# Kernel tuning notes

Hardware: AMD Instinct MI355X
Metric: run time of the kernel (lower is better)

## Reference

```python
import jax, jax.numpy as jnp
import numpy as np

E = 1024
H = 16
DH = E // H
LN_EPS = 1e-5


def setup_inputs() -> dict:
    key = jax.random.key(0)
    ks = jax.random.split(key, 9)
    B, Lq, Lk = 8, 1024, 1024
    s = 0.02
    return {
        "query": jax.random.normal(ks[0], (B, Lq, E), jnp.float32),
        "key_t": jax.random.normal(ks[1], (B, Lk, E), jnp.float32),
        "value": jax.random.normal(ks[2], (B, Lk, E), jnp.float32),
        "in_proj_w": jax.random.normal(ks[3], (3 * E, E), jnp.float32) * s,
        "in_proj_b": jnp.zeros((3 * E,), jnp.float32),
        "out_proj_w": jax.random.normal(ks[4], (E, E), jnp.float32) * s,
        "out_proj_b": jnp.zeros((E,), jnp.float32),
        "ln_gamma": jnp.ones((E,), jnp.float32),
        "ln_beta": jnp.zeros((E,), jnp.float32),
    }


def _mha_cross(query, key_t, value, in_proj_w, in_proj_b, out_proj_w, out_proj_b,
               ln_gamma, ln_beta):
    B, Lq, _ = query.shape
    Lk = key_t.shape[1]
    wq, wk, wv = in_proj_w[:E], in_proj_w[E:2 * E], in_proj_w[2 * E:]
    bq, bk, bv = in_proj_b[:E], in_proj_b[E:2 * E], in_proj_b[2 * E:]
    # projections (torch Linear: x @ W^T + b)
    q = (query @ wq.T + bq).reshape(B, Lq, H, DH)
    k = (key_t @ wk.T + bk).reshape(B, Lk, H, DH)
    v = (value @ wv.T + bv).reshape(B, Lk, H, DH)
    scale = 1.0 / np.sqrt(DH).astype(np.float32)
    # unfused attention: explicit [B,H,Lq,Lk] scores (need_weights=True path)
    scores = jnp.einsum("bqhd,bkhd->bhqk", q, k) * scale
    probs = jax.nn.softmax(scores, axis=-1)
    attn = jnp.einsum("bhqk,bkhd->bqhd", probs, v).reshape(B, Lq, E)
    attn_out = attn @ out_proj_w.T + out_proj_b
    # averaged attention weights (average_attn_weights=True default)
    attn_weights = probs.mean(axis=1)  # [B, Lq, Lk]
    # residual + LayerNorm
    x = query + attn_out
    mu = x.mean(axis=-1, keepdims=True)
    var = x.var(axis=-1, keepdims=True)
    y = (x - mu) * jax.lax.rsqrt(var + LN_EPS) * ln_gamma + ln_beta
    return y, attn_weights


def reference(query, key_t, value, in_proj_w, in_proj_b, out_proj_w, out_proj_b,
              ln_gamma, ln_beta):
    return _mha_cross(query, key_t, value, in_proj_w, in_proj_b,
                      out_proj_w, out_proj_b, ln_gamma, ln_beta)
```

## Files before the change

kernel.cpp:

```cpp
#include <hip/hip_runtime.h>
#include <stdint.h>

#define E_DIM 1024
#define H_NUM 16
#define B_NUM 8
#define LQ 1024
#define LK 1024
#define MROWS (B_NUM * LQ)

typedef unsigned short u16;
typedef __attribute__((ext_vector_type(8))) short bf16x8;
typedef __attribute__((ext_vector_type(4))) short bf16x4;
typedef __attribute__((ext_vector_type(4))) float f32x4;
typedef __attribute__((ext_vector_type(2))) unsigned int u32x2;
typedef bf16x8 __attribute__((may_alias)) bf16x8_ma;
typedef bf16x4 __attribute__((may_alias)) bf16x4_ma;
typedef f32x4 __attribute__((may_alias)) f32x4_ma;
typedef u32x2 __attribute__((may_alias)) u32x2_ma;

typedef __attribute__((address_space(1))) const void* gas_ptr;
typedef __attribute__((address_space(3))) void* las_ptr;

__device__ __forceinline__ void gload16(const void* g, void* l) {
  __builtin_amdgcn_global_load_lds((gas_ptr)g, (las_ptr)l, 16, 0, 0);
}

__device__ __forceinline__ u16 f2bf(float f) {
  union { float f; uint32_t u; } c; c.f = f;
  return (u16)((c.u + 0x7FFFu + ((c.u >> 16) & 1u)) >> 16);
}

__device__ __forceinline__ uint32_t pack2bf(float lo, float hi) {
  return __builtin_amdgcn_perm(__float_as_uint(hi), __float_as_uint(lo), 0x07060302u);
}

#define MFMA_BF16(a, b, c) __builtin_amdgcn_mfma_f32_16x16x32_bf16((a), (b), (c), 0, 0, 0)

#define SCALE_Q 0.18033688011112042f


__global__ __launch_bounds__(256) void cvt_f32_bf16(const float* __restrict__ src,
                                                    u16* __restrict__ dst, int n4) {
  int i = blockIdx.x * 256 + threadIdx.x;
  const int stride = gridDim.x * 256;
  for (; i < n4; i += stride) {
    float4 v = ((const float4*)src)[i];
    ushort4 o;
    o.x = f2bf(v.x); o.y = f2bf(v.y); o.z = f2bf(v.z); o.w = f2bf(v.w);
    ((ushort4*)dst)[i] = o;
  }
}

__global__ __launch_bounds__(256) void cvt3_f32_bf16(
    const float* __restrict__ a0, const float* __restrict__ a1, const float* __restrict__ a2,
    u16* __restrict__ o0, u16* __restrict__ o1, u16* __restrict__ o2, int n4) {
  const float* s = (blockIdx.y == 0) ? a0 : (blockIdx.y == 1 ? a1 : a2);
  u16* d = (blockIdx.y == 0) ? o0 : (blockIdx.y == 1 ? o1 : o2);
  int i = blockIdx.x * 256 + threadIdx.x;
  const int stride = gridDim.x * 256;
  for (; i < n4; i += stride) {
    float4 v = ((const float4*)s)[i];
    ushort4 o;
    o.x = f2bf(v.x); o.y = f2bf(v.y); o.z = f2bf(v.z); o.w = f2bf(v.w);
    ((ushort4*)d)[i] = o;
  }
}


#define BAR() __builtin_amdgcn_s_barrier()
#define LGKM0() do { asm volatile("s_waitcnt lgkmcnt(0)" ::: "memory"); \
                     __builtin_amdgcn_sched_barrier(0); } while (0)
#define LGKM8() asm volatile("s_waitcnt lgkmcnt(8)" ::: "memory")
#define VMC(n) asm volatile("s_waitcnt vmcnt(" n ")" ::: "memory")

#define STAGEH(mat, rowbase, kt, ldsoff)                                     \
  { const u16* _s = (mat) + (size_t)(rowbase) * E_DIM + (kt);                \
    gload16(_s + goff0, ldsv + (ldsoff) + wave * 1024);                      \
    gload16(_s + goff1, ldsv + (ldsoff) + 8192 + wave * 1024); }

#define READ_B(db)                                                           \
  _Pragma("unroll") for (int n = 0; n < 4; ++n) {                            \
    const int rgb = wn4 + n;                                                 \
    _Pragma("unroll") for (int ks = 0; ks < 2; ++ks)                         \
      bfr[n][ks] = *(const bf16x8_ma*)(ldsc + 65536 + (db) * 32768 +         \
          ((rgb >> 3) << 14) + (((rgb & 7) * 2 + ks) << 10) + lanebase);     \
  }

#define READ_A(db, q)                                                        \
  _Pragma("unroll") for (int jj = 0; jj < 2; ++jj) {                         \
    const int rga = 4 * (q) + 2 * jj + wm;                                   \
    _Pragma("unroll") for (int ks = 0; ks < 2; ++ks)                         \
      afr[jj][ks] = *(const bf16x8_ma*)(ldsc + (db) * 32768 +                \
          ((rga >> 3) << 14) + (((rga & 7) * 2 + ks) << 10) + lanebase);     \
  }

#define MMA(q)                                                               \
  __builtin_amdgcn_s_setprio(1);                                             \
  _Pragma("unroll") for (int jj = 0; jj < 2; ++jj)                           \
    _Pragma("unroll") for (int n = 0; n < 4; ++n)                            \
      _Pragma("unroll") for (int ks = 0; ks < 2; ++ks)                       \
        acc[2 * (q) + jj][n] =                                               \
            MFMA_BF16(afr[jj][ks], bfr[n][ks], acc[2 * (q) + jj][n]);        \
  __builtin_amdgcn_s_setprio(0);

template <int MODE>
__global__ __launch_bounds__(512, 2) void gemm256(
    const u16* __restrict__ A0, const u16* __restrict__ A1, const u16* __restrict__ A2,
    const u16* __restrict__ W, const float* __restrict__ bias,
    const float* __restrict__ resid,
    u16* __restrict__ outb, float* __restrict__ outf,
    int nwg_n, int nwg_m) {
  __shared__ u16 lds[65536];

  const int tid = threadIdx.x;
  const int wave = tid >> 6, lane = tid & 63;
  const int lr = lane & 15, lg = lane >> 4;
  const int wm = wave >> 2, wn4 = (wave & 3) * 4;

  const int cpx = (int)gridDim.x >> 3;
  const int bid = blockIdx.x;
  const int wg = (bid & 7) * cpx + (bid >> 3);
  const int n_i = wg % nwg_n;
  const int rest = wg / nwg_n;
  const int m_i = rest % nwg_m;
  const int z = rest / nwg_m;
  const int m0 = m_i * 256, n0 = n_i * 256;

  const u16* Az = (z == 0) ? A0 : (z == 1 ? A1 : A2);
  const u16* Wz = W + (size_t)z * E_DIM * E_DIM;
  const float* bs = bias + z * E_DIM;
  const float scale = (MODE == 0 && z == 0) ? SCALE_Q : 1.0f;

  int goff0, goff1;
  {
    const int X0 = wave * 1024 + lane * 16;
    const int L0 = X0 ^ (((X0 >> 9) & 1) << 5);
    goff0 = (((L0 >> 10) >> 1) * 16 + ((L0 >> 6) & 15)) * E_DIM +
            ((L0 >> 10) & 1) * 32 + ((L0 & 63) >> 1);
    const int X1 = 8192 + X0;
    const int L1 = X1 ^ (((X1 >> 9) & 1) << 5);
    goff1 = (((L1 >> 10) >> 1) * 16 + ((L1 >> 6) & 15)) * E_DIM +
            ((L1 >> 10) & 1) * 32 + ((L1 & 63) >> 1);
  }
  const char* ldsc = (const char*)lds;
  char* ldsv = (char*)lds;
  const int lanebase = lr * 64 + ((lg * 16) ^ ((lane & 8) << 2));

  const f32x4 fzero = {0.f, 0.f, 0.f, 0.f};
  f32x4 acc[8][4];
#pragma unroll
  for (int j = 0; j < 8; ++j)
#pragma unroll
    for (int n = 0; n < 4; ++n) acc[j][n] = fzero;

  STAGEH(Az, m0,       0,  0);
  STAGEH(Az, m0 + 128, 0,  16384);
  STAGEH(Wz, n0,       0,  65536);
  STAGEH(Wz, n0 + 128, 0,  65536 + 16384);
  STAGEH(Wz, n0,       64, 65536 + 32768);
  STAGEH(Wz, n0 + 128, 64, 65536 + 32768 + 16384);
  STAGEH(Az, m0,       64, 32768);
  VMC("6");
  BAR();

  bf16x8 bfr[4][2], afr[2][2];
#pragma unroll 1
  for (int i = 0; i < 8; ++i) {
    const int kt2 = i * 128 + 128;
    const bool nl = (i < 7);
    READ_B(0) READ_A(0, 0)
    STAGEH(Az, m0 + 128, i * 128 + 64, 32768 + 16384);
    LGKM8();
    BAR(); LGKM0();
    MMA(0)
    BAR();
    READ_A(0, 1)
    if (nl) STAGEH(Wz, n0, kt2, 65536);
    BAR(); LGKM0();
    MMA(1)
    BAR();
    READ_A(0, 2)
    if (nl) STAGEH(Az, m0, kt2, 0);
    BAR(); LGKM0();
    MMA(2)
    BAR();
    READ_A(0, 3)
    if (nl) {
      STAGEH(Wz, n0 + 128, kt2, 65536 + 16384);
      VMC("6");
    } else {
      VMC("0");
    }
    BAR(); LGKM0();
    MMA(3)
    BAR();
    READ_B(1) READ_A(1, 0)
    if (nl) STAGEH(Az, m0 + 128, kt2, 16384);
    LGKM8();
    BAR(); LGKM0();
    MMA(0)
    BAR();
    READ_A(1, 1)
    if (nl) STAGEH(Wz, n0, kt2 + 64, 65536 + 32768);
    BAR(); LGKM0();
    MMA(1)
    BAR();
    READ_A(1, 2)
    if (nl) STAGEH(Wz, n0 + 128, kt2 + 64, 65536 + 32768 + 16384);
    BAR(); LGKM0();
    MMA(2)
    BAR();
    READ_A(1, 3)
    if (nl) {
      STAGEH(Az, m0, kt2 + 64, 32768);
      VMC("6");
    }
    BAR(); LGKM0();
    MMA(3)
    BAR();
  }

  float bvv[4];
#pragma unroll
  for (int n = 0; n < 4; ++n) bvv[n] = bs[n0 + wn4 * 16 + n * 16 + lr];

  if (MODE == 0) {
    u16* Cb = outb + (size_t)z * (size_t)MROWS * E_DIM;
#pragma unroll
    for (int j = 0; j < 8; ++j) {
      const int rbase = m0 + (2 * j + wm) * 16 + lg * 4;
#pragma unroll
      for (int ii = 0; ii < 4; ++ii) {
        const size_t m = (size_t)(rbase + ii);
#pragma unroll
        for (int n = 0; n < 4; ++n) {
          const int nn = n0 + wn4 * 16 + n * 16 + lr;
          Cb[m * E_DIM + nn] = f2bf((acc[j][n][ii] + bvv[n]) * scale);
        }
      }
    }
  } else {
#pragma unroll
    for (int j = 0; j < 8; ++j) {
      const int rbase = m0 + (2 * j + wm) * 16 + lg * 4;
#pragma unroll
      for (int ii = 0; ii < 4; ++ii) {
        const size_t m = (size_t)(rbase + ii);
#pragma unroll
        for (int n = 0; n < 4; ++n) {
          const int nn = n0 + wn4 * 16 + n * 16 + lr;
          outf[m * E_DIM + nn] = acc[j][n][ii] + bvv[n] + resid[m * E_DIM + nn];
        }
      }
    }
  }
}

__global__ __launch_bounds__(256) void gemm128_out(
    const u16* __restrict__ A, const u16* __restrict__ W,
    const float* __restrict__ bias, const float* __restrict__ resid,
    float* __restrict__ outf, int nwg_n, int nwg_m) {
  __shared__ u16 As[128 * 64];
  __shared__ u16 Bs[128 * 64];

  const int tid = threadIdx.x;
  const int wave = tid >> 6;
  const int lane = tid & 63;
  const int lr = lane & 15, lg = lane >> 4;
  const int wr = wave >> 1, wc = wave & 1;

  const int cpx = (int)gridDim.x >> 3;
  const int bid = blockIdx.x;
  const int wg = (bid & 7) * cpx + (bid >> 3);
  const int n_i = wg % nwg_n;
  const int m_i = (wg / nwg_n) % nwg_m;

  const int m0 = m_i * 128;
  const int n0 = n_i * 128;

  const f32x4 fzero = {0.f, 0.f, 0.f, 0.f};
  f32x4 acc[4][4];
#pragma unroll
  for (int a = 0; a < 4; ++a)
#pragma unroll
    for (int b = 0; b < 4; ++b) acc[a][b] = fzero;

  const int lrow8 = lane >> 3;
  const int lcol8 = (lane & 7) * 8;

  for (int kt = 0; kt < E_DIM; kt += 64) {
#pragma unroll
    for (int i = 0; i < 4; ++i) {
      const int seg = i * 4 + wave;
      gload16(W + (size_t)(n0 + seg * 8 + lrow8) * E_DIM + kt + lcol8, &Bs[seg * 512]);
      gload16(A + (size_t)(m0 + seg * 8 + lrow8) * E_DIM + kt + lcol8, &As[seg * 512]);
    }
    __syncthreads();

#pragma unroll
    for (int kk = 0; kk < 64; kk += 32) {
      bf16x8 av[4], bv[4];
#pragma unroll
      for (int t = 0; t < 4; ++t)
        av[t] = *(const bf16x8*)&As[(wr * 64 + t * 16 + lr) * 64 + kk + lg * 8];
#pragma unroll
      for (int t = 0; t < 4; ++t)
        bv[t] = *(const bf16x8*)&Bs[(wc * 64 + t * 16 + lr) * 64 + kk + lg * 8];
#pragma unroll
      for (int mi = 0; mi < 4; ++mi)
#pragma unroll
        for (int ni = 0; ni < 4; ++ni)
          acc[mi][ni] = MFMA_BF16(av[mi], bv[ni], acc[mi][ni]);
    }
    __syncthreads();
  }

  float bvv[4];
#pragma unroll
  for (int ni = 0; ni < 4; ++ni) bvv[ni] = bias[n0 + wc * 64 + ni * 16 + lr];

#pragma unroll
  for (int mi = 0; mi < 4; ++mi) {
#pragma unroll
    for (int i = 0; i < 4; ++i) {
      const size_t m = (size_t)(m0 + wr * 64 + mi * 16 + lg * 4 + i);
#pragma unroll
      for (int ni = 0; ni < 4; ++ni) {
        const int n = n0 + wc * 64 + ni * 16 + lr;
        outf[m * E_DIM + n] = acc[mi][ni][i] + bvv[ni] + resid[m * E_DIM + n];
      }
    }
  }
}

__global__ __launch_bounds__(256) void transpose_v(const u16* __restrict__ Vb,
                                                   u16* __restrict__ Vtg) {
  __shared__ u16 T[64 * 264];
  const int tid = threadIdx.x;
  const int b = blockIdx.z, h = blockIdx.y;
  const int k0 = blockIdx.x * 256;
  const int bh = b * H_NUM + h;
  const int krow = tid >> 3;
  const int d0 = (tid & 7) * 8;
  const int jst = krow & 7;
#pragma unroll
  for (int it = 0; it < 8; ++it) {
    const int k = it * 32 + krow;
    bf16x8 v = *(const bf16x8*)&Vb[(size_t)(b * LK + k0 + k) * E_DIM + h * 64 + d0];
#pragma unroll
    for (int jj = 0; jj < 8; ++jj) {
      const int j = (jj + jst) & 7;
      T[(d0 + j) * 264 + k] = (u16)v[j];
    }
  }
  __syncthreads();
  const int d = tid >> 2;
  const int kk0 = (tid & 3) * 64;
  u16* orow = &Vtg[(size_t)(bh * 64 + d) * LK + k0 + kk0];
#pragma unroll
  for (int c = 0; c < 8; ++c)
    *(bf16x8*)&orow[c * 8] = *(const bf16x8*)&T[d * 264 + kk0 + c * 8];
}

__global__ __launch_bounds__(512) void attn_fwd(
    const u16* __restrict__ Qb, const u16* __restrict__ Kb, const u16* __restrict__ Vtg,
    u16* __restrict__ attnb, float* __restrict__ rden) {
  __shared__ u16 Ks[64 * 72];
  __shared__ u16 Vt[64 * 72];
  __shared__ u16 Pw[8][16 * 72];

  const int tid = threadIdx.x;
  const int wave = tid >> 6, lane = tid & 63;
  const int lr = lane & 15, lg = lane >> 4;

  const int bid = blockIdx.x;
  const int wg = (bid & 7) * 128 + (bid >> 3);
  const int qt = wg & 7;
  const int h = (wg >> 3) & 15;
  const int b = wg >> 7;
  const int bh = b * H_NUM + h;
  const int q0 = qt * 128;

  const size_t qoff = (size_t)(b * LQ + q0 + wave * 16 + lr) * E_DIM + h * 64;
  const bf16x8 qf0 = *(const bf16x8*)&Qb[qoff + lg * 8];
  const bf16x8 qf1 = *(const bf16x8*)&Qb[qoff + 32 + lg * 8];

  const f32x4 fzero = {0.f, 0.f, 0.f, 0.f};
  f32x4 ctx[4];
#pragma unroll
  for (int d = 0; d < 4; ++d) ctx[d] = fzero;
  float dnl = 0.f;

  const int sr = tid >> 3;
  const int sc = (tid & 7) * 8;
  const u16* Kg = &Kb[(size_t)(b * LK + sr) * E_DIM + h * 64 + sc];
  const u16* Vg = &Vtg[(size_t)(bh * 64 + sr) * LK + sc];

  bf16x8 kr = *(const bf16x8*)(Kg);
  bf16x8 vr = *(const bf16x8*)(Vg);
  *(bf16x8*)&Ks[sr * 72 + sc] = kr;
  *(bf16x8*)&Vt[sr * 72 + sc] = vr;

  for (int t = 0; t < 16; ++t) {
    __syncthreads();
    if (t < 15) {
      const int k1 = (t + 1) * 64;
      kr = *(const bf16x8*)(Kg + (size_t)k1 * E_DIM);
      vr = *(const bf16x8*)(Vg + k1);
    }
#pragma unroll
    for (int kf = 0; kf < 4; ++kf) {
      const bf16x8 kb0 = *(const bf16x8*)&Ks[(kf * 16 + lr) * 72 + lg * 8];
      const bf16x8 kb1 = *(const bf16x8*)&Ks[(kf * 16 + lr) * 72 + 32 + lg * 8];
      f32x4 s = fzero;
      s = MFMA_BF16(kb0, qf0, s);
      s = MFMA_BF16(kb1, qf1, s);
      const float p0 = exp2f(s[0]), p1 = exp2f(s[1]);
      const float p2 = exp2f(s[2]), p3 = exp2f(s[3]);
      dnl += (p0 + p1) + (p2 + p3);
      u32x2 w;
      w[0] = pack2bf(p0, p1);
      w[1] = pack2bf(p2, p3);
      *(u32x2_ma*)&Pw[wave][lr * 72 + kf * 16 + lg * 4] = w;
    }
    const bf16x8 pa0 = *(const bf16x8_ma*)&Pw[wave][lr * 72 + lg * 8];
    const bf16x8 pa1 = *(const bf16x8_ma*)&Pw[wave][lr * 72 + 32 + lg * 8];
#pragma unroll
    for (int df = 0; df < 4; ++df) {
      const bf16x8 vb0 = *(const bf16x8*)&Vt[(df * 16 + lr) * 72 + lg * 8];
      const bf16x8 vb1 = *(const bf16x8*)&Vt[(df * 16 + lr) * 72 + 32 + lg * 8];
      ctx[df] = MFMA_BF16(pa0, vb0, ctx[df]);
      ctx[df] = MFMA_BF16(pa1, vb1, ctx[df]);
    }
    __syncthreads();
    if (t < 15) {
      *(bf16x8*)&Ks[sr * 72 + sc] = kr;
      *(bf16x8*)&Vt[sr * 72 + sc] = vr;
    }
  }

  dnl += __shfl_xor(dnl, 16, 64);
  dnl += __shfl_xor(dnl, 32, 64);
  if (lane < 16) rden[(size_t)bh * LQ + q0 + wave * 16 + lane] = 0.0625f / dnl;
  float dnv[4];
#pragma unroll
  for (int i = 0; i < 4; ++i) dnv[i] = __shfl(dnl, lg * 4 + i, 64);

#pragma unroll
  for (int i = 0; i < 4; ++i) {
    const float inv = 1.0f / dnv[i];
    const int q = q0 + wave * 16 + lg * 4 + i;
    const size_t orow = (size_t)(b * LQ + q) * E_DIM + h * 64;
#pragma unroll
    for (int df = 0; df < 4; ++df)
      attnb[orow + df * 16 + lr] = f2bf(ctx[df][i] * inv);
  }
}

__global__ __launch_bounds__(256, 2) void attn_wts(
    const u16* __restrict__ Qb, const u16* __restrict__ Kb,
    const float* __restrict__ rden, float* __restrict__ aw) {
  __shared__ u16 Ks2[2][128 * 72];
  __shared__ u16 Qs[128 * 72];

  const int tid = threadIdx.x;
  const int wave = tid >> 6, lane = tid & 63;
  const int lr = lane & 15, lg = lane >> 4;
  const int wq = wave >> 1, wk = wave & 1;

  const int bid = blockIdx.x;
  const int wg = (bid & 7) * 64 + (bid >> 3);
  const int q0 = (wg & 7) * 128;
  const int k0 = ((wg >> 3) & 7) * 128;
  const int b = wg >> 6;

  const f32x4 fzero = {0.f, 0.f, 0.f, 0.f};
  f32x4 acc[4][4];
#pragma unroll
  for (int t = 0; t < 4; ++t)
#pragma unroll
    for (int j = 0; j < 4; ++j) acc[t][j] = fzero;

  const int sr = tid >> 1;
  const int sc = (tid & 1) * 32;
  const u16* Kg = &Kb[(size_t)(b * LK + k0 + sr) * E_DIM + sc];
  const u16* Qg = &Qb[(size_t)(b * LQ + q0 + sr) * E_DIM + sc];
  const float* dg = &rden[(size_t)(b * H_NUM) * LQ + q0 + wq * 64 + lr];

  bf16x8 kr[4], qr[4];
#pragma unroll
  for (int c = 0; c < 4; ++c) kr[c] = *(const bf16x8*)(Kg + c * 8);
#pragma unroll
  for (int c = 0; c < 4; ++c) qr[c] = *(const bf16x8*)(Qg + c * 8);
#pragma unroll
  for (int c = 0; c < 4; ++c) *(bf16x8*)&Ks2[0][sr * 72 + sc + c * 8] = kr[c];

  for (int h = 0; h < H_NUM; ++h) {
    __syncthreads();
#pragma unroll
    for (int c = 0; c < 4; ++c) *(bf16x8*)&Qs[sr * 72 + sc + c * 8] = qr[c];
    __syncthreads();

    if (h < 15) {
#pragma unroll
      for (int c = 0; c < 4; ++c) kr[c] = *(const bf16x8*)(Kg + (h + 1) * 64 + c * 8);
#pragma unroll
      for (int c = 0; c < 4; ++c) qr[c] = *(const bf16x8*)(Qg + (h + 1) * 64 + c * 8);
    }
    float rd[4];
#pragma unroll
    for (int j = 0; j < 4; ++j) rd[j] = dg[(size_t)h * LQ + j * 16];

    const u16* Kbuf = &Ks2[h & 1][0];
    bf16x8 kb[4][2];
#pragma unroll
    for (int t = 0; t < 4; ++t) {
      const int row = wk * 64 + t * 16 + lr;
      kb[t][0] = *(const bf16x8*)&Kbuf[row * 72 + lg * 8];
      kb[t][1] = *(const bf16x8*)&Kbuf[row * 72 + 32 + lg * 8];
    }
#pragma unroll
    for (int j = 0; j < 4; ++j) {
      const int qrow = wq * 64 + j * 16 + lr;
      const bf16x8 qf0 = *(const bf16x8*)&Qs[qrow * 72 + lg * 8];
      const bf16x8 qf1 = *(const bf16x8*)&Qs[qrow * 72 + 32 + lg * 8];
#pragma unroll
      for (int t = 0; t < 4; ++t) {
        f32x4 s = fzero;
        s = MFMA_BF16(kb[t][0], qf0, s);
        s = MFMA_BF16(kb[t][1], qf1, s);
#pragma unroll
        for (int i = 0; i < 4; ++i)
          acc[t][j][i] += exp2f(s[i]) * rd[j];
      }
    }

    if (h < 15) {
      u16* Kw = &Ks2[(h + 1) & 1][0];
#pragma unroll
      for (int c = 0; c < 4; ++c) *(bf16x8*)&Kw[sr * 72 + sc + c * 8] = kr[c];
    }
  }

#pragma unroll
  for (int j = 0; j < 4; ++j) {
    const size_t orow = (size_t)(b * LQ + q0 + wq * 64 + j * 16 + lr) * LK;
#pragma unroll
    for (int t = 0; t < 4; ++t)
      *(f32x4_ma*)&aw[orow + k0 + wk * 64 + t * 16 + lg * 4] = acc[t][j];
  }
}

__global__ __launch_bounds__(256) void ln_kernel(float* __restrict__ xy,
                                                 const float* __restrict__ gamma,
                                                 const float* __restrict__ beta) {
  __shared__ float ls[4], ls2[4];
  const int row = blockIdx.x;
  const int tid = threadIdx.x;
  float4* xr = (float4*)(xy + (size_t)row * E_DIM);
  float4 v = xr[tid];
  float s = v.x + v.y + v.z + v.w;
  float s2 = v.x * v.x + v.y * v.y + v.z * v.z + v.w * v.w;
#pragma unroll
  for (int off = 32; off >= 1; off >>= 1) {
    s += __shfl_xor(s, off, 64);
    s2 += __shfl_xor(s2, off, 64);
  }
  const int wave = tid >> 6, lane = tid & 63;
  if (lane == 0) { ls[wave] = s; ls2[wave] = s2; }
  __syncthreads();
  s = ls[0] + ls[1] + ls[2] + ls[3];
  s2 = ls2[0] + ls2[1] + ls2[2] + ls2[3];
  const float mu = s * (1.0f / E_DIM);
  const float var = s2 * (1.0f / E_DIM) - mu * mu;
  const float rs = rsqrtf(var + 1e-5f);
  const float4 g = ((const float4*)gamma)[tid];
  const float4 bt = ((const float4*)beta)[tid];
  float4 o;
  o.x = (v.x - mu) * rs * g.x + bt.x;
  o.y = (v.y - mu) * rs * g.y + bt.y;
  o.z = (v.z - mu) * rs * g.z + bt.z;
  o.w = (v.w - mu) * rs * g.w + bt.w;
  xr[tid] = o;
}

extern "C" void kernel_launch(void* const* d_in, const int* in_sizes, int n_in,
                              void* d_out, int out_size, void* d_ws, size_t ws_size,
                              hipStream_t stream) {
  (void)in_sizes; (void)n_in; (void)out_size; (void)ws_size;
  const float* query     = (const float*)d_in[0];
  const float* key_t     = (const float*)d_in[1];
  const float* value     = (const float*)d_in[2];
  const float* in_proj_b = (const float*)d_in[4];
  const float* out_proj_b = (const float*)d_in[6];
  const float* ln_gamma  = (const float*)d_in[7];
  const float* ln_beta   = (const float*)d_in[8];

  float* y  = (float*)d_out;
  float* aw = y + (size_t)B_NUM * LQ * E_DIM;

  const size_t SZ = (size_t)B_NUM * LQ * E_DIM;
  u16* ws    = (u16*)d_ws;
  u16* Qb    = ws;
  u16* Kb    = ws + SZ;
  u16* Vb    = ws + 2 * SZ;
  u16* attnb = ws + 3 * SZ;
  u16* wqkvb = ws + 4 * SZ;
  u16* woutb = wqkvb + 3 * E_DIM * E_DIM;
  float* rden = (float*)(wqkvb + 4 * (size_t)E_DIM * E_DIM);

  u16* Xq  = (u16*)aw;
  u16* Xk  = Xq + SZ;
  u16* Xv  = (u16*)y;
  u16* Vtg = (u16*)y;

  cvt_f32_bf16<<<3072, 256, 0, stream>>>((const float*)d_in[3], wqkvb, (3 * E_DIM * E_DIM) / 4);
  cvt_f32_bf16<<<1024, 256, 0, stream>>>((const float*)d_in[5], woutb, (E_DIM * E_DIM) / 4);
  cvt3_f32_bf16<<<dim3(2048, 3), 256, 0, stream>>>(query, key_t, value, Xq, Xk, Xv, (int)(SZ / 4));

  gemm256<0><<<384, 512, 0, stream>>>(
      Xq, Xk, Xv, wqkvb, in_proj_b, nullptr, Qb, nullptr, 4, 32);

  transpose_v<<<dim3(4, 16, 8), 256, 0, stream>>>(Vb, Vtg);

  attn_fwd<<<1024, 512, 0, stream>>>(Qb, Kb, Vtg, attnb, rden);

  attn_wts<<<512, 256, 0, stream>>>(Qb, Kb, rden, aw);

  gemm128_out<<<512, 256, 0, stream>>>(attnb, woutb, out_proj_b, query, y, 8, 64);

  ln_kernel<<<8192, 256, 0, stream>>>(y, ln_gamma, ln_beta);
}
```

Before: 258.1 us.

## Restructure QKV GEMM into 4-stage K=32 ring pipeline with XOR-swizzled LDS

The QKV projection GEMM now stages 32-wide K slices into a 4-deep LDS ring, three slices in flight, instead of the previous double-buffered K=64 halves. Global-to-LDS loads use a simpler per-thread row/column mapping with an XOR swizzle on the 16-byte chunk to avoid bank conflicts. The goal is deeper prefetch to better hide memory latency behind MFMA work. The catch is twice as many loop iterations, with more barriers and waits per unit of compute. The unused float-output template mode is dropped.

```diff
diff --git a/kernel.cpp b/kernel.cpp
--- a/kernel.cpp
+++ b/kernel.cpp
@@ -70,46 +70,38 @@
 #define BAR() __builtin_amdgcn_s_barrier()
 #define LGKM0() do { asm volatile("s_waitcnt lgkmcnt(0)" ::: "memory"); \
                      __builtin_amdgcn_sched_barrier(0); } while (0)
-#define LGKM8() asm volatile("s_waitcnt lgkmcnt(8)" ::: "memory")
 #define VMC(n) asm volatile("s_waitcnt vmcnt(" n ")" ::: "memory")
 
-#define STAGEH(mat, rowbase, kt, ldsoff)                                     \
-  { const u16* _s = (mat) + (size_t)(rowbase) * E_DIM + (kt);                \
-    gload16(_s + goff0, ldsv + (ldsoff) + wave * 1024);                      \
-    gload16(_s + goff1, ldsv + (ldsoff) + 8192 + wave * 1024); }
-
-#define READ_B(db)                                                           \
-  _Pragma("unroll") for (int n = 0; n < 4; ++n) {                            \
-    const int rgb = wn4 + n;                                                 \
-    _Pragma("unroll") for (int ks = 0; ks < 2; ++ks)                         \
-      bfr[n][ks] = *(const bf16x8_ma*)(ldsc + 65536 + (db) * 32768 +         \
-          ((rgb >> 3) << 14) + (((rgb & 7) * 2 + ks) << 10) + lanebase);     \
-  }
-
-#define READ_A(db, q)                                                        \
-  _Pragma("unroll") for (int jj = 0; jj < 2; ++jj) {                         \
-    const int rga = 4 * (q) + 2 * jj + wm;                                   \
-    _Pragma("unroll") for (int ks = 0; ks < 2; ++ks)                         \
-      afr[jj][ks] = *(const bf16x8_ma*)(ldsc + (db) * 32768 +                \
-          ((rga >> 3) << 14) + (((rga & 7) * 2 + ks) << 10) + lanebase);     \
-  }
-
-#define MMA(q)                                                               \
-  __builtin_amdgcn_s_setprio(1);                                             \
-  _Pragma("unroll") for (int jj = 0; jj < 2; ++jj)                           \
-    _Pragma("unroll") for (int n = 0; n < 4; ++n)                            \
-      _Pragma("unroll") for (int ks = 0; ks < 2; ++ks)                       \
-        acc[2 * (q) + jj][n] =                                               \
-            MFMA_BF16(afr[jj][ks], bfr[n][ks], acc[2 * (q) + jj][n]);        \
+#define ST_A0(t) gload16(pA0 + (size_t)(t) * 32, ldsv + ((t) & 3) * 16384 + wave * 1024)
+#define ST_A1(t) gload16(pA1 + (size_t)(t) * 32, ldsv + ((t) & 3) * 16384 + 8192 + wave * 1024)
+#define ST_B0(t) gload16(pB0 + (size_t)(t) * 32, ldsv + 65536 + ((t) & 3) * 16384 + wave * 1024)
+#define ST_B1(t) gload16(pB1 + (size_t)(t) * 32, ldsv + 65536 + ((t) & 3) * 16384 + 8192 + wave * 1024)
+
+#define RD_A(buf, q)                                                          \
+  _Pragma("unroll") for (int jj = 0; jj < 2; ++jj) {                          \
+    const int rg = 4 * (q) + 2 * jj + wm;                                     \
+    const int rh = (rg & 7) * 16 + lr;                                        \
+    afr[jj] = *(const bf16x8_ma*)(ldsc + (buf) * 16384 + ((rg >> 3) << 13) +  \
+                                  rh * 64 + rchunk);                          \
+  }
+#define RD_B(buf)                                                             \
+  _Pragma("unroll") for (int n = 0; n < 4; ++n) {                             \
+    const int rg = wn4 + n;                                                   \
+    const int rh = (rg & 7) * 16 + lr;                                        \
+    bfr[n] = *(const bf16x8_ma*)(ldsc + 65536 + (buf) * 16384 +               \
+                                 ((rg >> 3) << 13) + rh * 64 + rchunk);       \
+  }
+#define MMA32(q)                                                              \
+  __builtin_amdgcn_s_setprio(1);                                              \
+  _Pragma("unroll") for (int jj = 0; jj < 2; ++jj)                            \
+    _Pragma("unroll") for (int n = 0; n < 4; ++n)                             \
+      acc[2 * (q) + jj][n] = MFMA_BF16(afr[jj], bfr[n], acc[2 * (q) + jj][n]);\
   __builtin_amdgcn_s_setprio(0);
 
-template <int MODE>
-__global__ __launch_bounds__(512, 2) void gemm256(
+__global__ __launch_bounds__(512, 2) void gemm_qkv(
     const u16* __restrict__ A0, const u16* __restrict__ A1, const u16* __restrict__ A2,
     const u16* __restrict__ W, const float* __restrict__ bias,
-    const float* __restrict__ resid,
-    u16* __restrict__ outb, float* __restrict__ outf,
-    int nwg_n, int nwg_m) {
+    u16* __restrict__ outb, int nwg_n, int nwg_m) {
   __shared__ u16 lds[65536];
 
   const int tid = threadIdx.x;
@@ -129,22 +121,17 @@
   const u16* Az = (z == 0) ? A0 : (z == 1 ? A1 : A2);
   const u16* Wz = W + (size_t)z * E_DIM * E_DIM;
   const float* bs = bias + z * E_DIM;
-  const float scale = (MODE == 0 && z == 0) ? SCALE_Q : 1.0f;
-
-  int goff0, goff1;
-  {
-    const int X0 = wave * 1024 + lane * 16;
-    const int L0 = X0 ^ (((X0 >> 9) & 1) << 5);
-    goff0 = (((L0 >> 10) >> 1) * 16 + ((L0 >> 6) & 15)) * E_DIM +
-            ((L0 >> 10) & 1) * 32 + ((L0 & 63) >> 1);
-    const int X1 = 8192 + X0;
-    const int L1 = X1 ^ (((X1 >> 9) & 1) << 5);
-    goff1 = (((L1 >> 10) >> 1) * 16 + ((L1 >> 6) & 15)) * E_DIM +
-            ((L1 >> 10) & 1) * 32 + ((L1 & 63) >> 1);
-  }
+  const float scale = (z == 0) ? SCALE_Q : 1.0f;
+
+  const int grow = tid >> 2;
+  const int gcol = ((tid & 3) ^ ((tid >> 2) & 3) ^ ((tid >> 4) & 3)) * 8;
+  const u16* pA0 = Az + (size_t)(m0 + grow) * E_DIM + gcol;
+  const u16* pA1 = Az + (size_t)(m0 + 128 + grow) * E_DIM + gcol;
+  const u16* pB0 = Wz + (size_t)(n0 + grow) * E_DIM + gcol;
+  const u16* pB1 = Wz + (size_t)(n0 + 128 + grow) * E_DIM + gcol;
+  char* ldsv = (char*)lds;
   const char* ldsc = (const char*)lds;
-  char* ldsv = (char*)lds;
-  const int lanebase = lr * 64 + ((lg * 16) ^ ((lane & 8) << 2));
+  const int rchunk = ((lg ^ (lr & 3) ^ ((lr >> 2) & 3)) << 4);
 
   const f32x4 fzero = {0.f, 0.f, 0.f, 0.f};
   f32x4 acc[8][4];
@@ -153,70 +140,58 @@
 #pragma unroll
     for (int n = 0; n < 4; ++n) acc[j][n] = fzero;
 
-  STAGEH(Az, m0,       0,  0);
-  STAGEH(Az, m0 + 128, 0,  16384);
-  STAGEH(Wz, n0,       0,  65536);
-  STAGEH(Wz, n0 + 128, 0,  65536 + 16384);
-  STAGEH(Wz, n0,       64, 65536 + 32768);
-  STAGEH(Wz, n0 + 128, 64, 65536 + 32768 + 16384);
-  STAGEH(Az, m0,       64, 32768);
-  VMC("6");
+#pragma unroll
+  for (int t = 0; t < 3; ++t) { ST_A0(t); ST_A1(t); ST_B0(t); ST_B1(t); }
+  VMC("8");
   BAR();
 
-  bf16x8 bfr[4][2], afr[2][2];
+  bf16x8 afr[2], bfr[4];
 #pragma unroll 1
-  for (int i = 0; i < 8; ++i) {
-    const int kt2 = i * 128 + 128;
-    const bool nl = (i < 7);
-    READ_B(0) READ_A(0, 0)
-    STAGEH(Az, m0 + 128, i * 128 + 64, 32768 + 16384);
-    LGKM8();
-    BAR(); LGKM0();
-    MMA(0)
-    BAR();
-    READ_A(0, 1)
-    if (nl) STAGEH(Wz, n0, kt2, 65536);
-    BAR(); LGKM0();
-    MMA(1)
-    BAR();
-    READ_A(0, 2)
-    if (nl) STAGEH(Az, m0, kt2, 0);
-    BAR(); LGKM0();
-    MMA(2)
-    BAR();
-    READ_A(0, 3)
-    if (nl) {
-      STAGEH(Wz, n0 + 128, kt2, 65536 + 16384);
-      VMC("6");
-    } else {
-      VMC("0");
-    }
-    BAR(); LGKM0();
-    MMA(3)
-    BAR();
-    READ_B(1) READ_A(1, 0)
-    if (nl) STAGEH(Az, m0 + 128, kt2, 16384);
-    LGKM8();
-    BAR(); LGKM0();
-    MMA(0)
-    BAR();
-    READ_A(1, 1)
-    if (nl) STAGEH(Wz, n0, kt2 + 64, 65536 + 32768);
-    BAR(); LGKM0();
-    MMA(1)
-    BAR();
-    READ_A(1, 2)
-    if (nl) STAGEH(Wz, n0 + 128, kt2 + 64, 65536 + 32768 + 16384);
-    BAR(); LGKM0();
-    MMA(2)
-    BAR();
-    READ_A(1, 3)
-    if (nl) {
-      STAGEH(Az, m0, kt2 + 64, 32768);
-      VMC("6");
-    }
-    BAR(); LGKM0();
-    MMA(3)
+  for (int i = 0; i < 16; ++i) {
+    const int r0 = (2 * i) & 3, r1 = (2 * i + 1) & 3;
+    const int ts0 = 2 * i + 3, ts1 = 2 * i + 4;
+    const bool s0 = (i <= 14), s1 = (i <= 13);
+    RD_B(r0) RD_A(r0, 0)
+    if (s0) ST_A0(ts0);
+    BAR(); LGKM0();
+    MMA32(0)
+    BAR();
+    RD_A(r0, 1)
+    if (s0) ST_A1(ts0);
+    BAR(); LGKM0();
+    MMA32(1)
+    BAR();
+    RD_A(r0, 2)
+    if (s0) ST_B0(ts0);
+    BAR(); LGKM0();
+    MMA32(2)
+    BAR();
+    RD_A(r0, 3)
+    if (s0) ST_B1(ts0);
+    BAR(); LGKM0();
+    MMA32(3)
+    if (i <= 14) { VMC("8"); } else { VMC("0"); }
+    BAR();
+    RD_B(r1) RD_A(r1, 0)
+    if (s1) ST_A0(ts1);
+    BAR(); LGKM0();
+    MMA32(0)
+    BAR();
+    RD_A(r1, 1)
+    if (s1) ST_A1(ts1);
+    BAR(); LGKM0();
+    MMA32(1)
+    BAR();
+    RD_A(r1, 2)
+    if (s1) ST_B0(ts1);
+    BAR(); LGKM0();
+    MMA32(2)
+    BAR();
+    RD_A(r1, 3)
+    if (s1) ST_B1(ts1);
+    BAR(); LGKM0();
+    MMA32(3)
+    if (i <= 13) { VMC("8"); } else if (i == 14) { VMC("4"); }
     BAR();
   }
 
@@ -224,33 +199,17 @@
 #pragma unroll
   for (int n = 0; n < 4; ++n) bvv[n] = bs[n0 + wn4 * 16 + n * 16 + lr];
 
-  if (MODE == 0) {
-    u16* Cb = outb + (size_t)z * (size_t)MROWS * E_DIM;
-#pragma unroll
-    for (int j = 0; j < 8; ++j) {
-      const int rbase = m0 + (2 * j + wm) * 16 + lg * 4;
-#pragma unroll
-      for (int ii = 0; ii < 4; ++ii) {
-        const size_t m = (size_t)(rbase + ii);
-#pragma unroll
-        for (int n = 0; n < 4; ++n) {
-          const int nn = n0 + wn4 * 16 + n * 16 + lr;
-          Cb[m * E_DIM + nn] = f2bf((acc[j][n][ii] + bvv[n]) * scale);
-        }
-      }
-    }
-  } else {
-#pragma unroll
-    for (int j = 0; j < 8; ++j) {
-      const int rbase = m0 + (2 * j + wm) * 16 + lg * 4;
-#pragma unroll
-      for (int ii = 0; ii < 4; ++ii) {
-        const size_t m = (size_t)(rbase + ii);
-#pragma unroll
-        for (int n = 0; n < 4; ++n) {
-          const int nn = n0 + wn4 * 16 + n * 16 + lr;
-          outf[m * E_DIM + nn] = acc[j][n][ii] + bvv[n] + resid[m * E_DIM + nn];
-        }
+  u16* Cb = outb + (size_t)z * (size_t)MROWS * E_DIM;
+#pragma unroll
+  for (int j = 0; j < 8; ++j) {
+    const int rbase = m0 + (2 * j + wm) * 16 + lg * 4;
+#pragma unroll
+    for (int ii = 0; ii < 4; ++ii) {
+      const size_t m = (size_t)(rbase + ii);
+#pragma unroll
+      for (int n = 0; n < 4; ++n) {
+        const int nn = n0 + wn4 * 16 + n * 16 + lr;
+        Cb[m * E_DIM + nn] = f2bf((acc[j][n][ii] + bvv[n]) * scale);
       }
     }
   }
@@ -618,8 +577,8 @@
   cvt_f32_bf16<<<1024, 256, 0, stream>>>((const float*)d_in[5], woutb, (E_DIM * E_DIM) / 4);
   cvt3_f32_bf16<<<dim3(2048, 3), 256, 0, stream>>>(query, key_t, value, Xq, Xk, Xv, (int)(SZ / 4));
 
-  gemm256<0><<<384, 512, 0, stream>>>(
-      Xq, Xk, Xv, wqkvb, in_proj_b, nullptr, Qb, nullptr, 4, 32);
+  gemm_qkv<<<384, 512, 0, stream>>>(
+      Xq, Xk, Xv, wqkvb, in_proj_b, Qb, 4, 32);
 
   transpose_v<<<dim3(4, 16, 8), 256, 0, stream>>>(Vb, Vtg);
 
```

Result: slower. 269.2 us (+4.3%).
